# Kernel optimization log

Hardware: AMD Instinct MI355X
Metric: run time of the kernel (lower is better)

Reference implementation:

```python
import jax, jax.numpy as jnp
import numpy as np

B, C, D, T, N_SUBJ = 64, 1024, 1024, 1024, 32


def setup_inputs() -> dict:
    key = jax.random.key(0)
    k1, k2, k3 = jax.random.split(key, 3)
    x = jax.random.normal(k1, (B, C, T), dtype=jnp.float32)
    subjects = jax.random.randint(k2, (B,), 0, N_SUBJ, dtype=jnp.int64)
    # weights: normal_() then scaled by 1/sqrt(in_channels), as in __init__
    weights = jax.random.normal(k3, (N_SUBJ, C, D), dtype=jnp.float32) / np.sqrt(C).astype(np.float32)
    return {"x": x, "subjects": subjects, "weights": weights}


def reference(x, subjects, weights):
    # gather per-sample projection matrices: (B, C, D)
    w = weights[subjects]
    # out[b, d, t] = sum_c x[b, c, t] * w[b, c, d]
    return jnp.einsum('bct,bcd->bdt', x, w)
```

## Files before the change

kernel.cpp:

```cpp
#include <hip/hip_runtime.h>
#include <hip/hip_bf16.h>

typedef __attribute__((ext_vector_type(8))) short bf16x8;
typedef __attribute__((ext_vector_type(4))) float f32x4;
typedef __attribute__((ext_vector_type(4))) unsigned u32x4;

#define CDIM 1024
#define DDIM 1024
#define TDIM 1024
#define BK 32

__device__ __forceinline__ unsigned cvt_pk_bf16(float a, float b) {
    unsigned r;
    asm("v_cvt_pk_bf16_f32 %0, %1, %2" : "=v"(r) : "v"(a), "v"(b));
    return r;
}
__device__ __forceinline__ int swz8(int r) { return (r ^ (r >> 3)) & 7; }
__device__ __forceinline__ int swz4(int r) { return (r ^ (r >> 3)) & 3; }

__global__ __launch_bounds__(512, 1)
void prep_w(const float* __restrict__ w, short* __restrict__ wopt)
{
    __shared__ float T[32 * 260];
    const int blk = blockIdx.x;
    const int kt = blk & 31;
    const int dt = (blk >> 5) & 3;
    const int s  = blk >> 7;
    const float* wb = w + (size_t)s * (CDIM * DDIM)
                        + (size_t)(kt * 32) * DDIM + dt * 256;
    const int tid = threadIdx.x;
    {
        const int row = tid >> 4;
        const int seg = tid & 15;
        const float* src = wb + (size_t)row * DDIM + seg * 16;
        float4 a0 = *(const float4*)(src);
        float4 a1 = *(const float4*)(src + 4);
        float4 a2 = *(const float4*)(src + 8);
        float4 a3 = *(const float4*)(src + 12);
        float* dst = T + row * 260 + seg * 16;
        *(float4*)(dst) = a0;      *(float4*)(dst + 4) = a1;
        *(float4*)(dst + 8) = a2;  *(float4*)(dst + 12) = a3;
    }
    __syncthreads();
    short* outc = wopt + (size_t)blk * 16384;
    #pragma unroll
    for (int j = 0; j < 4; ++j) {
        const int u = tid + 512 * j;
        const int r = u >> 3;
        const int sl = u & 7;
        const int g = sl ^ swz8(r);
        const int kk = (g & 3) * 8;
        const bool hi = (g < 4);
        unsigned o[4];
        #pragma unroll
        for (int p = 0; p < 4; ++p) {
            const float f0 = T[(kk + 2 * p    ) * 260 + r];
            const float f1 = T[(kk + 2 * p + 1) * 260 + r];
            const unsigned h = cvt_pk_bf16(f0, f1);
            const float l0 = f0 - __uint_as_float(h << 16);
            const float l1 = f1 - __uint_as_float(h & 0xFFFF0000u);
            const unsigned lo = cvt_pk_bf16(l0, l1);
            o[p] = hi ? h : lo;
        }
        *(u32x4*)(outc + (size_t)u * 8) = *(u32x4*)o;
    }
}

#define KSTEP(P, Q, KNEXT)                                                      \
  {                                                                             \
    const int kn = (KNEXT) & (CDIM - 1);                                        \
    _Pragma("unroll")                                                           \
    for (int j = 0; j < 4; ++j)                                                 \
        v[j] = *(const float4*)(xp + ((size_t)(kn + cbase + j) << 10));         \
    {                                                                           \
      const short* gsrc = wchunk + (size_t)(kn >> 5) * 16384                    \
                          + wave * 2048 + lane * 8;                             \
      short* ldst = &Wt[Q][wave * 2048];                                        \
      _Pragma("unroll")                                                         \
      for (int q = 0; q < 4; ++q)                                               \
        __builtin_amdgcn_global_load_lds(                                       \
            (const __attribute__((address_space(1))) void*)(gsrc + q * 512),    \
            (__attribute__((address_space(3))) void*)(ldst + q * 512),          \
            16, 0, 0);                                                          \
    }                                                                           \
    asm volatile("s_waitcnt vmcnt(8)" ::: "memory");                            \
    __builtin_amdgcn_sched_barrier(0);                                          \
    {                                                                           \
      bf16x8 ah[4], al[4];                                                      \
      _Pragma("unroll")                                                         \
      for (int m = 0; m < 4; ++m) {                                             \
        const short* wrow = &Wt[P][(wdOff + m * 16 + fr) * 64];                 \
        ah[m] = *(const bf16x8*)(wrow + offHW[m]);                              \
        al[m] = *(const bf16x8*)(wrow + (offHW[m] ^ 32));                       \
      }                                                                         \
      _Pragma("unroll")                                                         \
      for (int np = 0; np < 4; ++np) {                                          \
        const int n0 = 2 * np, n1 = 2 * np + 1;                                 \
        const bf16x8 bh0 = *(const bf16x8*)(&Xt[P][(wtOff + n0 * 16 + fr) * 32] + offHX[n0]); \
        const bf16x8 bh1 = *(const bf16x8*)(&Xt[P][(wtOff + n1 * 16 + fr) * 32] + offHX[n1]); \
        _Pragma("unroll")                                                       \
        for (int m = 0; m < 4; ++m)                                             \
          acc[m][n0] = __builtin_amdgcn_mfma_f32_16x16x32_bf16(ah[m], bh0, acc[m][n0], 0, 0, 0); \
        _Pragma("unroll")                                                       \
        for (int m = 0; m < 4; ++m)                                             \
          acc[m][n1] = __builtin_amdgcn_mfma_f32_16x16x32_bf16(ah[m], bh1, acc[m][n1], 0, 0, 0); \
        _Pragma("unroll")                                                       \
        for (int m = 0; m < 4; ++m)                                             \
          acc[m][n0] = __builtin_amdgcn_mfma_f32_16x16x32_bf16(al[m], bh0, acc[m][n0], 0, 0, 0); \
        _Pragma("unroll")                                                       \
        for (int m = 0; m < 4; ++m)                                             \
          acc[m][n1] = __builtin_amdgcn_mfma_f32_16x16x32_bf16(al[m], bh1, acc[m][n1], 0, 0, 0); \
      }                                                                         \
    }                                                                           \
    asm volatile("s_waitcnt vmcnt(4)" ::: "memory");                            \
    __builtin_amdgcn_sched_barrier(0);                                          \
    _Pragma("unroll")                                                           \
    for (int rr = 0; rr < 4; ++rr) {                                            \
      const unsigned h0 = cvt_pk_bf16(v[0][rr], v[1][rr]);                      \
      const unsigned h1 = cvt_pk_bf16(v[2][rr], v[3][rr]);                      \
      const int row = col0 + rr;                                                \
      const int so = ((xg ^ swz4(row)) << 3) + xh * 4;                          \
      uint2 pr; pr.x = h0; pr.y = h1;                                           \
      *(uint2*)(&Xt[Q][row * 32 + so]) = pr;                                    \
    }                                                                           \
    asm volatile("s_waitcnt lgkmcnt(0)" ::: "memory");                          \
    __builtin_amdgcn_sched_barrier(0);                                          \
    __builtin_amdgcn_s_barrier();                                               \
    __builtin_amdgcn_sched_barrier(0);                                          \
  }

__global__ __launch_bounds__(512, 1)
void subject_gemm2(const float* __restrict__ x, const int* __restrict__ subj,
                   const short* __restrict__ wopt, float* __restrict__ out)
{
    __shared__ short Wt[2][256 * 64];
    __shared__ short Xt[2][256 * 32];

    const int bid = blockIdx.x;
    const int xcd = bid & 7;
    const int slot = bid >> 3;
    const int b = (xcd << 3) | (slot >> 4);
    const int r = slot & 15;
    const int dtIdx = r >> 2;
    const int dtile = dtIdx << 8;
    const int ttile = (r & 3) << 8;

    const int s = subj[b];
    const short* __restrict__ wchunk = wopt + (size_t)((s * 4 + dtIdx) * 32) * 16384;
    const float* __restrict__ xB = x + (size_t)b * (CDIM * TDIM);

    const int tid = threadIdx.x;
    const int lane = tid & 63;
    const int wave = tid >> 6;

    const int tq = tid & 63;
    const int cg = tid >> 6;
    const int xg = cg >> 1;
    const int xh = cg & 1;
    const int cbase = cg * 4;
    const int col0 = tq * 4;
    const float* xp = xB + ttile + col0;

    const int wdOff = (wave >> 1) << 6;
    const int wtOff = (wave & 1) << 7;
    const int fr = lane & 15;
    const int fg = lane >> 4;

    int offHW[4], offHX[8];
    #pragma unroll
    for (int m = 0; m < 4; ++m) {
        const int rowW = wdOff + m * 16 + fr;
        offHW[m] = ((fg ^ swz8(rowW)) << 3);
    }
    #pragma unroll
    for (int n = 0; n < 8; ++n) {
        const int rowX = wtOff + n * 16 + fr;
        offHX[n] = ((fg ^ swz4(rowX)) << 3);
    }

    f32x4 acc[4][8] = {};
    float4 v[4];

    #pragma unroll
    for (int j = 0; j < 4; ++j)
        v[j] = *(const float4*)(xp + ((size_t)(cbase + j) << 10));
    asm volatile("s_waitcnt vmcnt(0)" ::: "memory");
    __builtin_amdgcn_sched_barrier(0);
    #pragma unroll
    for (int rr = 0; rr < 4; ++rr) {
        const unsigned h0 = cvt_pk_bf16(v[0][rr], v[1][rr]);
        const unsigned h1 = cvt_pk_bf16(v[2][rr], v[3][rr]);
        const int row = col0 + rr;
        const int so = ((xg ^ swz4(row)) << 3) + xh * 4;
        uint2 pr; pr.x = h0; pr.y = h1;
        *(uint2*)(&Xt[0][row * 32 + so]) = pr;
    }
    {
        const short* gsrc = wchunk + wave * 2048 + lane * 8;
        short* ldst = &Wt[0][wave * 2048];
        #pragma unroll
        for (int q = 0; q < 4; ++q)
            __builtin_amdgcn_global_load_lds(
                (const __attribute__((address_space(1))) void*)(gsrc + q * 512),
                (__attribute__((address_space(3))) void*)(ldst + q * 512),
                16, 0, 0);
    }
    asm volatile("s_waitcnt lgkmcnt(0)" ::: "memory");
    __builtin_amdgcn_sched_barrier(0);
    __builtin_amdgcn_s_barrier();
    __builtin_amdgcn_sched_barrier(0);

    for (int k0 = 0; k0 < CDIM; k0 += 2 * BK) {
        KSTEP(0, 1, k0 + BK);
        KSTEP(1, 0, k0 + 2 * BK);
    }

    float* __restrict__ oB = out + (size_t)b * (DDIM * TDIM)
                           + (size_t)(dtile + wdOff) * TDIM + (ttile + wtOff);
    #pragma unroll
    for (int m = 0; m < 4; ++m) {
        #pragma unroll
        for (int q = 0; q < 4; ++q) {
            const int d = m * 16 + (fg << 2) + q;
            float* orow = oB + (size_t)d * TDIM;
            #pragma unroll
            for (int n = 0; n < 8; ++n) {
                orow[n * 16 + fr] = acc[m][n][q];
            }
        }
    }
}

#define FKSTEP(VCUR, VNXT, K0)                                                  \
  {                                                                             \
    const int ksafe = ((K0) + BK) & (CDIM - 1);                                 \
    _Pragma("unroll")                                                           \
    for (int j = 0; j < 8; ++j)                                                 \
        VNXT[j] = *(const float4*)(sp + ((size_t)(ksafe + (cg << 3) + j) << 10)); \
    u32x4 hg[4], lg[4];                                                         \
    _Pragma("unroll")                                                           \
    for (int rr = 0; rr < 4; ++rr) {                                            \
      _Pragma("unroll")                                                         \
      for (int p = 0; p < 4; ++p) {                                             \
        const float f0 = VCUR[2 * p][rr];                                       \
        const float f1 = VCUR[2 * p + 1][rr];                                   \
        const unsigned h = cvt_pk_bf16(f0, f1);                                 \
        const float l0 = f0 - __uint_as_float(h << 16);                         \
        const float l1 = f1 - __uint_as_float(h & 0xFFFF0000u);                 \
        hg[rr][p] = h;                                                          \
        lg[rr][p] = cvt_pk_bf16(l0, l1);                                        \
      }                                                                         \
    }                                                                           \
    __syncthreads();                                                            \
    _Pragma("unroll")                                                           \
    for (int rr = 0; rr < 4; ++rr) {                                            \
      const int row = col0 + rr;                                                \
      short* sl = slds + row * 64;                                              \
      const int so = ((cg ^ swz8(row)) << 3);                                   \
      *(u32x4*)(sl + so) = hg[rr];                                              \
      *(u32x4*)(sl + (so ^ 32)) = lg[rr];                                       \
    }                                                                           \
    __syncthreads();                                                            \
    bf16x8 ah[4], al[4];                                                        \
    _Pragma("unroll")                                                           \
    for (int m = 0; m < 4; ++m) {                                               \
      const short* wrow = Wt + (wdOff + m * 16 + fr) * 64;                      \
      ah[m] = *(const bf16x8*)(wrow + offHW[m]);                                \
      al[m] = *(const bf16x8*)(wrow + (offHW[m] ^ 32));                         \
    }                                                                           \
    _Pragma("unroll")                                                           \
    for (int np = 0; np < 4; ++np) {                                            \
      const int n0 = 2 * np, n1 = 2 * np + 1;                                   \
      const short* xr0 = Xt + (wtOff + n0 * 16 + fr) * 64;                      \
      const short* xr1 = Xt + (wtOff + n1 * 16 + fr) * 64;                      \
      const bf16x8 bh0 = *(const bf16x8*)(xr0 + offHX[n0]);                     \
      const bf16x8 bl0 = *(const bf16x8*)(xr0 + (offHX[n0] ^ 32));              \
      const bf16x8 bh1 = *(const bf16x8*)(xr1 + offHX[n1]);                     \
      const bf16x8 bl1 = *(const bf16x8*)(xr1 + (offHX[n1] ^ 32));              \
      _Pragma("unroll")                                                         \
      for (int m = 0; m < 4; ++m)                                               \
        acc[m][n0] = __builtin_amdgcn_mfma_f32_16x16x32_bf16(ah[m], bh0, acc[m][n0], 0, 0, 0); \
      _Pragma("unroll")                                                         \
      for (int m = 0; m < 4; ++m)                                               \
        acc[m][n1] = __builtin_amdgcn_mfma_f32_16x16x32_bf16(ah[m], bh1, acc[m][n1], 0, 0, 0); \
      _Pragma("unroll")                                                         \
      for (int m = 0; m < 4; ++m)                                               \
        acc[m][n0] = __builtin_amdgcn_mfma_f32_16x16x32_bf16(ah[m], bl0, acc[m][n0], 0, 0, 0); \
      _Pragma("unroll")                                                         \
      for (int m = 0; m < 4; ++m)                                               \
        acc[m][n1] = __builtin_amdgcn_mfma_f32_16x16x32_bf16(ah[m], bl1, acc[m][n1], 0, 0, 0); \
      _Pragma("unroll")                                                         \
      for (int m = 0; m < 4; ++m)                                               \
        acc[m][n0] = __builtin_amdgcn_mfma_f32_16x16x32_bf16(al[m], bh0, acc[m][n0], 0, 0, 0); \
      _Pragma("unroll")                                                         \
      for (int m = 0; m < 4; ++m)                                               \
        acc[m][n1] = __builtin_amdgcn_mfma_f32_16x16x32_bf16(al[m], bh1, acc[m][n1], 0, 0, 0); \
    }                                                                           \
  }

__global__ __launch_bounds__(512, 1)
void subject_gemm_fb(const float* __restrict__ x, const int* __restrict__ subj,
                     const float* __restrict__ w, float* __restrict__ out)
{
    __shared__ short Wt[256 * 64];
    __shared__ short Xt[256 * 64];

    const int bid = blockIdx.x;
    const int xcd = bid & 7;
    const int slot = bid >> 3;
    const int b = (xcd << 3) | (slot >> 4);
    const int r = slot & 15;
    const int dtile = (r >> 2) << 8;
    const int ttile = (r & 3) << 8;

    const int s = subj[b];
    const float* __restrict__ wB = w + (size_t)s * (CDIM * DDIM);
    const float* __restrict__ xB = x + (size_t)b * (CDIM * TDIM);

    const int tid = threadIdx.x;
    const int lane = tid & 63;
    const int wave = tid >> 6;

    const int ht = tid & 255;
    const int tq = ht & 63;
    const int cg = ht >> 6;
    const int col0 = tq << 2;
    const bool isW = (tid < 256);
    const float* sp = (isW ? wB + dtile : xB + ttile) + col0;
    short* slds = (isW ? Wt : Xt);

    const int wdOff = (wave >> 1) << 6;
    const int wtOff = (wave & 1) << 7;
    const int fr = lane & 15;
    const int fg = lane >> 4;

    int offHW[4], offHX[8];
    #pragma unroll
    for (int m = 0; m < 4; ++m) {
        const int rowW = wdOff + m * 16 + fr;
        offHW[m] = ((fg ^ swz8(rowW)) << 3);
    }
    #pragma unroll
    for (int n = 0; n < 8; ++n) {
        const int rowX = wtOff + n * 16 + fr;
        offHX[n] = ((fg ^ swz8(rowX)) << 3);
    }

    f32x4 acc[4][8] = {};

    float4 va[8], vb[8];
    #pragma unroll
    for (int j = 0; j < 8; ++j)
        va[j] = *(const float4*)(sp + ((size_t)((cg << 3) + j) << 10));

    for (int k0 = 0; k0 < CDIM; k0 += 2 * BK) {
        FKSTEP(va, vb, k0);
        FKSTEP(vb, va, k0 + BK);
    }

    float* __restrict__ oB = out + (size_t)b * (DDIM * TDIM)
                           + (size_t)(dtile + wdOff) * TDIM + (ttile + wtOff);
    #pragma unroll
    for (int m = 0; m < 4; ++m) {
        #pragma unroll
        for (int q = 0; q < 4; ++q) {
            const int d = m * 16 + (fg << 2) + q;
            float* orow = oB + (size_t)d * TDIM;
            #pragma unroll
            for (int n = 0; n < 8; ++n) {
                orow[n * 16 + fr] = acc[m][n][q];
            }
        }
    }
}

extern "C" void kernel_launch(void* const* d_in, const int* in_sizes, int n_in,
                              void* d_out, int out_size, void* d_ws, size_t ws_size,
                              hipStream_t stream) {
    const float* x = (const float*)d_in[0];
    const int* subjects = (const int*)d_in[1];
    const float* w = (const float*)d_in[2];
    float* out = (float*)d_out;
    const size_t NEED = (size_t)4096 * 32768;
    if (ws_size >= NEED) {
        prep_w<<<dim3(4096), dim3(512), 0, stream>>>(w, (short*)d_ws);
        subject_gemm2<<<dim3(1024), dim3(512), 0, stream>>>(
            x, subjects, (const short*)d_ws, out);
    } else {
        subject_gemm_fb<<<dim3(1024), dim3(512), 0, stream>>>(x, subjects, w, out);
    }
}
```

Measured before the change: 385.3 us.

## Pre-convert x to swizzled bf16 in a separate kernel and DMA it into LDS

Adds a prep_x kernel that converts x to bf16 in a swizzled tile layout in the workspace. The GEMM then loads X tiles with global_load_lds, the same way as W, instead of doing float4 loads, conversion and LDS writes in the main loop. The K-step is also reordered: wait and barrier, read all fragments into registers, barrier, then run the MFMAs. The cost is an extra pass over x (read fp32, write bf16, then reread), a larger workspace requirement, and an extra barrier per step.

```diff
diff --git a/kernel.cpp b/kernel.cpp
--- a/kernel.cpp
+++ b/kernel.cpp
@@ -66,72 +66,102 @@
     }
 }
 
+__global__ __launch_bounds__(256, 2)
+void prep_x(const float* __restrict__ x, short* __restrict__ xopt)
+{
+    __shared__ float T[32 * 260];
+    const int blk = blockIdx.x;
+    const int kt = blk & 31;
+    const int tt = (blk >> 5) & 3;
+    const int b  = blk >> 7;
+    const float* xb = x + (size_t)b * (CDIM * TDIM)
+                        + (size_t)(kt * 32) * TDIM + tt * 256;
+    const int tid = threadIdx.x;
+    {
+        const int row = tid >> 3;
+        const int seg = tid & 7;
+        const float* src = xb + (size_t)row * TDIM + seg * 32;
+        float* dst = T + row * 260 + seg * 32;
+        #pragma unroll
+        for (int i = 0; i < 8; ++i)
+            *(float4*)(dst + i * 4) = *(const float4*)(src + i * 4);
+    }
+    __syncthreads();
+    short* outc = xopt + (size_t)blk * 8192;
+    #pragma unroll
+    for (int j = 0; j < 4; ++j) {
+        const int u = tid + 256 * j;
+        const int r = u >> 2;
+        const int sl = u & 3;
+        const int g = sl ^ swz4(r);
+        const int kk = g * 8;
+        unsigned o[4];
+        #pragma unroll
+        for (int p = 0; p < 4; ++p)
+            o[p] = cvt_pk_bf16(T[(kk + 2 * p) * 260 + r],
+                               T[(kk + 2 * p + 1) * 260 + r]);
+        *(u32x4*)(outc + (size_t)u * 8) = *(u32x4*)o;
+    }
+}
+
 #define KSTEP(P, Q, KNEXT)                                                      \
   {                                                                             \
     const int kn = (KNEXT) & (CDIM - 1);                                        \
-    _Pragma("unroll")                                                           \
-    for (int j = 0; j < 4; ++j)                                                 \
-        v[j] = *(const float4*)(xp + ((size_t)(kn + cbase + j) << 10));         \
     {                                                                           \
-      const short* gsrc = wchunk + (size_t)(kn >> 5) * 16384                    \
-                          + wave * 2048 + lane * 8;                             \
-      short* ldst = &Wt[Q][wave * 2048];                                        \
+      const short* gw = wchunk + (size_t)(kn >> 5) * 16384 + wave * 2048 + lane * 8; \
+      short* lw = &Wt[Q][wave * 2048];                                          \
       _Pragma("unroll")                                                         \
       for (int q = 0; q < 4; ++q)                                               \
         __builtin_amdgcn_global_load_lds(                                       \
-            (const __attribute__((address_space(1))) void*)(gsrc + q * 512),    \
-            (__attribute__((address_space(3))) void*)(ldst + q * 512),          \
-            16, 0, 0);                                                          \
-    }                                                                           \
-    asm volatile("s_waitcnt vmcnt(8)" ::: "memory");                            \
+            (const __attribute__((address_space(1))) void*)(gw + q * 512),      \
+            (__attribute__((address_space(3))) void*)(lw + q * 512), 16, 0, 0); \
+      const short* gx = xchunk + (size_t)(kn >> 5) * 8192 + wave * 1024 + lane * 8; \
+      short* lx = &Xt[Q][wave * 1024];                                          \
+      _Pragma("unroll")                                                         \
+      for (int q = 0; q < 2; ++q)                                               \
+        __builtin_amdgcn_global_load_lds(                                       \
+            (const __attribute__((address_space(1))) void*)(gx + q * 512),      \
+            (__attribute__((address_space(3))) void*)(lx + q * 512), 16, 0, 0); \
+    }                                                                           \
+    asm volatile("s_waitcnt vmcnt(6)" ::: "memory");                            \
     __builtin_amdgcn_sched_barrier(0);                                          \
-    {                                                                           \
-      bf16x8 ah[4], al[4];                                                      \
-      _Pragma("unroll")                                                         \
-      for (int m = 0; m < 4; ++m) {                                             \
-        const short* wrow = &Wt[P][(wdOff + m * 16 + fr) * 64];                 \
-        ah[m] = *(const bf16x8*)(wrow + offHW[m]);                              \
-        al[m] = *(const bf16x8*)(wrow + (offHW[m] ^ 32));                       \
-      }                                                                         \
-      _Pragma("unroll")                                                         \
-      for (int np = 0; np < 4; ++np) {                                          \
-        const int n0 = 2 * np, n1 = 2 * np + 1;                                 \
-        const bf16x8 bh0 = *(const bf16x8*)(&Xt[P][(wtOff + n0 * 16 + fr) * 32] + offHX[n0]); \
-        const bf16x8 bh1 = *(const bf16x8*)(&Xt[P][(wtOff + n1 * 16 + fr) * 32] + offHX[n1]); \
-        _Pragma("unroll")                                                       \
-        for (int m = 0; m < 4; ++m)                                             \
-          acc[m][n0] = __builtin_amdgcn_mfma_f32_16x16x32_bf16(ah[m], bh0, acc[m][n0], 0, 0, 0); \
-        _Pragma("unroll")                                                       \
-        for (int m = 0; m < 4; ++m)                                             \
-          acc[m][n1] = __builtin_amdgcn_mfma_f32_16x16x32_bf16(ah[m], bh1, acc[m][n1], 0, 0, 0); \
-        _Pragma("unroll")                                                       \
-        for (int m = 0; m < 4; ++m)                                             \
-          acc[m][n0] = __builtin_amdgcn_mfma_f32_16x16x32_bf16(al[m], bh0, acc[m][n0], 0, 0, 0); \
-        _Pragma("unroll")                                                       \
-        for (int m = 0; m < 4; ++m)                                             \
-          acc[m][n1] = __builtin_amdgcn_mfma_f32_16x16x32_bf16(al[m], bh1, acc[m][n1], 0, 0, 0); \
-      }                                                                         \
-    }                                                                           \
-    asm volatile("s_waitcnt vmcnt(4)" ::: "memory");                            \
+    __builtin_amdgcn_s_barrier();                                               \
     __builtin_amdgcn_sched_barrier(0);                                          \
-    _Pragma("unroll")                                                           \
-    for (int rr = 0; rr < 4; ++rr) {                                            \
-      const unsigned h0 = cvt_pk_bf16(v[0][rr], v[1][rr]);                      \
-      const unsigned h1 = cvt_pk_bf16(v[2][rr], v[3][rr]);                      \
-      const int row = col0 + rr;                                                \
-      const int so = ((xg ^ swz4(row)) << 3) + xh * 4;                          \
-      uint2 pr; pr.x = h0; pr.y = h1;                                           \
-      *(uint2*)(&Xt[Q][row * 32 + so]) = pr;                                    \
-    }                                                                           \
+    bf16x8 ah[4], al[4], bh[8];                                                 \
+    _Pragma("unroll")                                                           \
+    for (int m = 0; m < 4; ++m) {                                               \
+      const short* wrow = &Wt[P][(wdOff + m * 16 + fr) * 64];                   \
+      ah[m] = *(const bf16x8*)(wrow + offHW[m]);                                \
+      al[m] = *(const bf16x8*)(wrow + (offHW[m] ^ 32));                         \
+    }                                                                           \
+    _Pragma("unroll")                                                           \
+    for (int n = 0; n < 8; ++n)                                                 \
+      bh[n] = *(const bf16x8*)(&Xt[P][(wtOff + n * 16 + fr) * 32] + offHX[n]);  \
     asm volatile("s_waitcnt lgkmcnt(0)" ::: "memory");                          \
     __builtin_amdgcn_sched_barrier(0);                                          \
     __builtin_amdgcn_s_barrier();                                               \
     __builtin_amdgcn_sched_barrier(0);                                          \
+    _Pragma("unroll")                                                           \
+    for (int np = 0; np < 4; ++np) {                                            \
+      const int n0 = 2 * np, n1 = 2 * np + 1;                                   \
+      _Pragma("unroll")                                                         \
+      for (int m = 0; m < 4; ++m)                                               \
+        acc[m][n0] = __builtin_amdgcn_mfma_f32_16x16x32_bf16(ah[m], bh[n0], acc[m][n0], 0, 0, 0); \
+      _Pragma("unroll")                                                         \
+      for (int m = 0; m < 4; ++m)                                               \
+        acc[m][n1] = __builtin_amdgcn_mfma_f32_16x16x32_bf16(ah[m], bh[n1], acc[m][n1], 0, 0, 0); \
+      _Pragma("unroll")                                                         \
+      for (int m = 0; m < 4; ++m)                                               \
+        acc[m][n0] = __builtin_amdgcn_mfma_f32_16x16x32_bf16(al[m], bh[n0], acc[m][n0], 0, 0, 0); \
+      _Pragma("unroll")                                                         \
+      for (int m = 0; m < 4; ++m)                                               \
+        acc[m][n1] = __builtin_amdgcn_mfma_f32_16x16x32_bf16(al[m], bh[n1], acc[m][n1], 0, 0, 0); \
+    }                                                                           \
   }
 
 __global__ __launch_bounds__(512, 1)
-void subject_gemm2(const float* __restrict__ x, const int* __restrict__ subj,
-                   const short* __restrict__ wopt, float* __restrict__ out)
+void subject_gemm3(const int* __restrict__ subj, const short* __restrict__ wopt,
+                   const short* __restrict__ xopt, float* __restrict__ out)
 {
     __shared__ short Wt[2][256 * 64];
     __shared__ short Xt[2][256 * 32];
@@ -142,24 +172,17 @@
     const int b = (xcd << 3) | (slot >> 4);
     const int r = slot & 15;
     const int dtIdx = r >> 2;
+    const int ttIdx = r & 3;
     const int dtile = dtIdx << 8;
-    const int ttile = (r & 3) << 8;
+    const int ttile = ttIdx << 8;
 
     const int s = subj[b];
     const short* __restrict__ wchunk = wopt + (size_t)((s * 4 + dtIdx) * 32) * 16384;
-    const float* __restrict__ xB = x + (size_t)b * (CDIM * TDIM);
+    const short* __restrict__ xchunk = xopt + (size_t)((b * 4 + ttIdx) * 32) * 8192;
 
     const int tid = threadIdx.x;
     const int lane = tid & 63;
     const int wave = tid >> 6;
-
-    const int tq = tid & 63;
-    const int cg = tid >> 6;
-    const int xg = cg >> 1;
-    const int xh = cg & 1;
-    const int cbase = cg * 4;
-    const int col0 = tq * 4;
-    const float* xp = xB + ttile + col0;
 
     const int wdOff = (wave >> 1) << 6;
     const int wtOff = (wave & 1) << 7;
@@ -179,33 +202,24 @@
     }
 
     f32x4 acc[4][8] = {};
-    float4 v[4];
-
-    #pragma unroll
-    for (int j = 0; j < 4; ++j)
-        v[j] = *(const float4*)(xp + ((size_t)(cbase + j) << 10));
-    asm volatile("s_waitcnt vmcnt(0)" ::: "memory");
-    __builtin_amdgcn_sched_barrier(0);
-    #pragma unroll
-    for (int rr = 0; rr < 4; ++rr) {
-        const unsigned h0 = cvt_pk_bf16(v[0][rr], v[1][rr]);
-        const unsigned h1 = cvt_pk_bf16(v[2][rr], v[3][rr]);
-        const int row = col0 + rr;
-        const int so = ((xg ^ swz4(row)) << 3) + xh * 4;
-        uint2 pr; pr.x = h0; pr.y = h1;
-        *(uint2*)(&Xt[0][row * 32 + so]) = pr;
-    }
+
     {
-        const short* gsrc = wchunk + wave * 2048 + lane * 8;
-        short* ldst = &Wt[0][wave * 2048];
+        const short* gw = wchunk + wave * 2048 + lane * 8;
+        short* lw = &Wt[0][wave * 2048];
         #pragma unroll
         for (int q = 0; q < 4; ++q)
             __builtin_amdgcn_global_load_lds(
-                (const __attribute__((address_space(1))) void*)(gsrc + q * 512),
-                (__attribute__((address_space(3))) void*)(ldst + q * 512),
-                16, 0, 0);
-    }
-    asm volatile("s_waitcnt lgkmcnt(0)" ::: "memory");
+                (const __attribute__((address_space(1))) void*)(gw + q * 512),
+                (__attribute__((address_space(3))) void*)(lw + q * 512), 16, 0, 0);
+        const short* gx = xchunk + wave * 1024 + lane * 8;
+        short* lx = &Xt[0][wave * 1024];
+        #pragma unroll
+        for (int q = 0; q < 2; ++q)
+            __builtin_amdgcn_global_load_lds(
+                (const __attribute__((address_space(1))) void*)(gx + q * 512),
+                (__attribute__((address_space(3))) void*)(lx + q * 512), 16, 0, 0);
+    }
+    asm volatile("s_waitcnt vmcnt(0)" ::: "memory");
     __builtin_amdgcn_sched_barrier(0);
     __builtin_amdgcn_s_barrier();
     __builtin_amdgcn_sched_barrier(0);
@@ -381,11 +395,14 @@
     const int* subjects = (const int*)d_in[1];
     const float* w = (const float*)d_in[2];
     float* out = (float*)d_out;
-    const size_t NEED = (size_t)4096 * 32768;
-    if (ws_size >= NEED) {
-        prep_w<<<dim3(4096), dim3(512), 0, stream>>>(w, (short*)d_ws);
-        subject_gemm2<<<dim3(1024), dim3(512), 0, stream>>>(
-            x, subjects, (const short*)d_ws, out);
+    const size_t NEED_W = (size_t)4096 * 32768;
+    const size_t NEED_FULL = NEED_W + (size_t)8192 * 16384;
+    short* wopt = (short*)d_ws;
+    short* xopt = (short*)d_ws + (size_t)4096 * 16384;
+    if (ws_size >= NEED_FULL) {
+        prep_w<<<dim3(4096), dim3(512), 0, stream>>>(w, wopt);
+        prep_x<<<dim3(8192), dim3(256), 0, stream>>>(x, xopt);
+        subject_gemm3<<<dim3(1024), dim3(512), 0, stream>>>(subjects, wopt, xopt, out);
     } else {
         subject_gemm_fb<<<dim3(1024), dim3(512), 0, stream>>>(x, subjects, w, out);
     }
```

New measurement: 405.0 us. +5.1%, slower.
